# Kernel optimization log

Measured on AMD Instinct MI355X. Metric: run time of the kernel, lower is better.

Reference implementation:

```python
import jax, jax.numpy as jnp
import numpy as np

T, B, D, S, H, OUT = 365, 2048, 32, 27, 256, 1

def _glorot(key, shape):
    fan_in, fan_out = shape[1], shape[0]
    std = jnp.sqrt(2.0 / (fan_in + fan_out))
    return std * jax.random.normal(key, shape, dtype=jnp.float32)

def setup_inputs() -> dict:
    key = jax.random.key(0)
    ks = jax.random.split(key, 9)
    x_dd = jax.random.normal(ks[0], (T, B, D), dtype=jnp.float32)
    x_s = jax.random.normal(ks[1], (B, S), dtype=jnp.float32)
    weight_ih = _glorot(ks[2], (3 * H, D))
    weight_hh = _glorot(ks[3], (3 * H, H))
    bias = jnp.zeros((3 * H,), dtype=jnp.float32)
    w_in = _glorot(ks[4], (H, S))
    b_in = jnp.zeros((H,), dtype=jnp.float32)
    w_dense = _glorot(ks[5], (OUT, H))
    b_dense = jnp.zeros((OUT,), dtype=jnp.float32)
    return {"x_dd": x_dd, "x_s": x_s, "weight_ih": weight_ih,
            "weight_hh": weight_hh, "bias": bias, "w_in": w_in,
            "b_in": b_in, "w_dense": w_dense, "b_dense": b_dense}

def reference(x_dd, x_s, weight_ih, weight_hh, bias, w_in, b_in, w_dense, b_dense):
    # static input gate, computed once per sample: (B, H)
    i = jax.nn.sigmoid(x_s @ w_in.T + b_in)
    # precompute input projections for all timesteps: (T, B, 3H)
    x_proj = jnp.einsum('tbd,gd->tbg', x_dd, weight_ih) + bias

    def step(state, xp):
        h, c = state
        gates = xp + h @ weight_hh.T  # (B, 3H)
        f, g, o = jnp.split(gates, 3, axis=-1)
        f = jax.nn.sigmoid(f)
        g = jnp.tanh(g)
        o = jax.nn.sigmoid(o)
        c = f * c + i * g
        h = o * jnp.tanh(c)
        return (h, c), None

    init = (jnp.zeros((B, H), dtype=x_dd.dtype), jnp.zeros((B, H), dtype=x_dd.dtype))
    (h_final, _), _ = jax.lax.scan(step, init, x_proj)
    return h_final @ w_dense.T + b_dense  # (B, OUT)
```

## Files before the change

### kernel.cpp

```cpp
#include <hip/hip_runtime.h>

#define TT   365
#define BTOT 2048
#define DIN  32
#define SIN  27
#define HD   256
#define G3   768
#define BLOCK 512
#define ZBUF 4608
#define XOFF 4096
#define WIHL_OFF 9216
#define WHH7_OFF (WIHL_OFF + G3*64)
#define SMEM_SZ  (WHH7_OFF + G3*64)
#define L2E  1.442695040888963f

#define WS_WIH  (G3*HD*2)
#define WS_BIAS (WS_WIH + G3*DIN*2)

typedef float  f32x4  __attribute__((ext_vector_type(4)));
typedef short  bf16x8 __attribute__((ext_vector_type(8)));
typedef unsigned int u32x2 __attribute__((ext_vector_type(2)));

__device__ __forceinline__ unsigned short f2bf(float f) {
  unsigned u = __builtin_bit_cast(unsigned, f);
  u += 0x7fffu + ((u >> 16) & 1u);
  return (unsigned short)(u >> 16);
}
__device__ __forceinline__ float bf2f(unsigned short u) {
  unsigned v = ((unsigned)u) << 16;
  return __builtin_bit_cast(float, v);
}

__global__ void prep_kernel(const float* __restrict__ whh, const float* __restrict__ wih,
                            const float* __restrict__ bias,
                            unsigned short* __restrict__ whh_bf,
                            unsigned short* __restrict__ wih_bf,
                            float* __restrict__ bias_s) {
  int stride = gridDim.x * blockDim.x;
  int i0 = blockIdx.x * blockDim.x + threadIdx.x;
  for (int i = i0; i < G3 * HD; i += stride) {
    int row = i >> 8;
    float s = (row >= HD && row < 2 * HD) ? 2.0f * L2E : L2E;
    whh_bf[i] = f2bf(whh[i] * s);
  }
  for (int i = i0; i < G3 * DIN; i += stride) {
    int row = i >> 5;
    float s = (row >= HD && row < 2 * HD) ? 2.0f * L2E : L2E;
    wih_bf[i] = f2bf(wih[i] * s);
  }
  for (int i = i0; i < G3; i += stride) {
    float s = (i >= HD && i < 2 * HD) ? 2.0f * L2E : L2E;
    bias_s[i] = bias[i] * s;
  }
}

__global__ void __launch_bounds__(BLOCK, 2)
ealstm_kernel(const float* __restrict__ x_dd, const float* __restrict__ x_s,
              const float* __restrict__ w_in, const float* __restrict__ b_in,
              const float* __restrict__ w_dense, const float* __restrict__ b_dense,
              const unsigned short* __restrict__ whh_bf,
              const unsigned short* __restrict__ wih_bf,
              const float* __restrict__ bias_s,
              float* __restrict__ out) {
  __shared__ __attribute__((aligned(16))) char sm[SMEM_SZ];
  char* zb    = sm;
  char* wihl  = sm + WIHL_OFF;
  char* whh7l = sm + WHH7_OFF;

  const int tid  = threadIdx.x;
  const int b0   = blockIdx.x * 8;
  const int w    = tid >> 6;
  const int lane = tid & 63;
  const int m    = lane & 15;
  const int q    = lane >> 4;
  const int b    = m & 7;
  const int half = m >> 3;

  for (int i = tid; i < G3 * 4; i += BLOCK) {
    int row = i >> 2, qq = i & 3;
    int rot = ((qq + ((row >> 1) & 3)) & 3) << 4;
    *(bf16x8*)(wihl + row * 64 + rot)  = *(const bf16x8*)(wih_bf + row * DIN + qq * 8);
    *(bf16x8*)(whh7l + row * 64 + rot) =
        *(const bf16x8*)(whh_bf + (size_t)row * HD + 7 * 32 + qq * 8);
  }
  if (tid < 256) *(f32x4*)(zb + tid * 16) = f32x4{0.f, 0.f, 0.f, 0.f};

  const bool xthr = tid < 256;
  const int xr_ = (tid >> 5) & 7, xd = tid & 31;
  const int xso = XOFF + xr_ * 64 + ((((xd >> 3) + (xr_ >> 1)) & 3) << 4) + (xd & 7) * 2;
  const float* xq = x_dd + (size_t)(b0 + xr_) * DIN + xd;
  if (xthr) *(unsigned short*)(zb + xso) = f2bf(xq[0]);
  xq += (size_t)BTOT * DIN;

  const int sb0 = w * 16;
  int sbs[6];
  bf16x8 wr[6][7];
  #pragma unroll
  for (int s = 0; s < 6; ++s) {
    int sbase = sb0 + (s >= 3 ? 128 : 0) + (s % 3) * 256;
    sbs[s] = sbase;
    const unsigned short* wp = whh_bf + (size_t)(sbase + m) * HD + q * 8;
    #pragma unroll
    for (int kk = 0; kk < 7; ++kk) wr[s][kk] = *(const bf16x8*)(wp + kk * 32);
  }
  #pragma unroll
  for (int s = 0; s < 6; ++s)
    #pragma unroll
    for (int kk = 0; kk < 7; ++kk)
      asm volatile("" : "+v"(wr[s][kk]));

  const int j0 = sb0 + half * 128 + q * 4;
  float cst[4], ig[4];
  #pragma unroll
  for (int r = 0; r < 4; ++r) {
    int j = j0 + r;
    float a = b_in[j];
    const float* xr = x_s + (size_t)(b0 + b) * SIN;
    const float* wn = w_in + (size_t)j * SIN;
    #pragma unroll
    for (int ss = 0; ss < SIN; ++ss) a += xr[ss] * wn[ss];
    ig[r] = __builtin_amdgcn_rcpf(1.0f + __builtin_amdgcn_exp2f(-a * L2E));
    cst[r] = 0.0f;
  }

  const int swz = b << 4;
  const int wro = ((q + ((m >> 1) & 3)) & 3) << 4;
  const int xrd = XOFF + b * 64 + (((q + (b >> 1)) & 3) << 4);
  const int hrb = b * 512;
  const int hq  = q * 16;
  const int hw  = b * 512 + ((j0 * 2) ^ swz);
  const float* bfp = bias_s + j0;
  const float* bgp = bias_s + 256 + j0;
  const float* bop = bias_s + 512 + j0;

  const f32x4 z4 = f32x4{0.f, 0.f, 0.f, 0.f};
  __syncthreads();

  for (int t = 0; t < TT; ++t) {
    char* zc = zb + (t & 1) * ZBUF;
    char* zn = zb + ((t + 1) & 1) * ZBUF;

    float xv = 0.0f;
    if (xthr && t + 1 < TT) xv = xq[0];
    f32x4 bf4 = *(const f32x4*)bfp;
    f32x4 bg4 = *(const f32x4*)bgp;
    f32x4 bo4 = *(const f32x4*)bop;

    bf16x8 xf = *(const bf16x8*)(zc + xrd);
    f32x4 acc0, acc1, acc2, acc3, acc4, acc5;
    {
      bf16x8 w0 = *(const bf16x8*)(wihl + (sbs[0] + m) * 64 + wro);
      bf16x8 w1 = *(const bf16x8*)(wihl + (sbs[1] + m) * 64 + wro);
      bf16x8 w2 = *(const bf16x8*)(wihl + (sbs[2] + m) * 64 + wro);
      bf16x8 w3 = *(const bf16x8*)(wihl + (sbs[3] + m) * 64 + wro);
      bf16x8 w4 = *(const bf16x8*)(wihl + (sbs[4] + m) * 64 + wro);
      bf16x8 w5 = *(const bf16x8*)(wihl + (sbs[5] + m) * 64 + wro);
      acc0 = __builtin_amdgcn_mfma_f32_16x16x32_bf16(w0, xf, z4, 0, 0, 0);
      acc1 = __builtin_amdgcn_mfma_f32_16x16x32_bf16(w1, xf, z4, 0, 0, 0);
      acc2 = __builtin_amdgcn_mfma_f32_16x16x32_bf16(w2, xf, z4, 0, 0, 0);
      acc3 = __builtin_amdgcn_mfma_f32_16x16x32_bf16(w3, xf, z4, 0, 0, 0);
      acc4 = __builtin_amdgcn_mfma_f32_16x16x32_bf16(w4, xf, z4, 0, 0, 0);
      acc5 = __builtin_amdgcn_mfma_f32_16x16x32_bf16(w5, xf, z4, 0, 0, 0);
    }
    #pragma unroll
    for (int kk = 0; kk < 7; ++kk) {
      bf16x8 hf = *(const bf16x8*)(zc + hrb + ((kk * 64 + hq) ^ swz));
      acc0 = __builtin_amdgcn_mfma_f32_16x16x32_bf16(wr[0][kk], hf, acc0, 0, 0, 0);
      acc1 = __builtin_amdgcn_mfma_f32_16x16x32_bf16(wr[1][kk], hf, acc1, 0, 0, 0);
      acc2 = __builtin_amdgcn_mfma_f32_16x16x32_bf16(wr[2][kk], hf, acc2, 0, 0, 0);
      acc3 = __builtin_amdgcn_mfma_f32_16x16x32_bf16(wr[3][kk], hf, acc3, 0, 0, 0);
      acc4 = __builtin_amdgcn_mfma_f32_16x16x32_bf16(wr[4][kk], hf, acc4, 0, 0, 0);
      acc5 = __builtin_amdgcn_mfma_f32_16x16x32_bf16(wr[5][kk], hf, acc5, 0, 0, 0);
    }
    {
      bf16x8 hf = *(const bf16x8*)(zc + hrb + ((7 * 64 + hq) ^ swz));
      bf16x8 u0 = *(const bf16x8*)(whh7l + (sbs[0] + m) * 64 + wro);
      bf16x8 u1 = *(const bf16x8*)(whh7l + (sbs[1] + m) * 64 + wro);
      bf16x8 u2 = *(const bf16x8*)(whh7l + (sbs[2] + m) * 64 + wro);
      bf16x8 u3 = *(const bf16x8*)(whh7l + (sbs[3] + m) * 64 + wro);
      bf16x8 u4 = *(const bf16x8*)(whh7l + (sbs[4] + m) * 64 + wro);
      bf16x8 u5 = *(const bf16x8*)(whh7l + (sbs[5] + m) * 64 + wro);
      acc0 = __builtin_amdgcn_mfma_f32_16x16x32_bf16(u0, hf, acc0, 0, 0, 0);
      acc1 = __builtin_amdgcn_mfma_f32_16x16x32_bf16(u1, hf, acc1, 0, 0, 0);
      acc2 = __builtin_amdgcn_mfma_f32_16x16x32_bf16(u2, hf, acc2, 0, 0, 0);
      acc3 = __builtin_amdgcn_mfma_f32_16x16x32_bf16(u3, hf, acc3, 0, 0, 0);
      acc4 = __builtin_amdgcn_mfma_f32_16x16x32_bf16(u4, hf, acc4, 0, 0, 0);
      acc5 = __builtin_amdgcn_mfma_f32_16x16x32_bf16(u5, hf, acc5, 0, 0, 0);
    }

    float h0, h1, h2, h3;
    #pragma unroll
    for (int r = 0; r < 4; ++r) {
      float pf = (half ? acc3[r] : acc0[r]) + bf4[r];
      float pg = (half ? acc4[r] : acc1[r]) + bg4[r];
      float po = (half ? acc5[r] : acc2[r]) + bo4[r];
      float fg = __builtin_amdgcn_rcpf(1.0f + __builtin_amdgcn_exp2f(-pf));
      float gg = 1.0f - 2.0f * __builtin_amdgcn_rcpf(1.0f + __builtin_amdgcn_exp2f(pg));
      float og = __builtin_amdgcn_rcpf(1.0f + __builtin_amdgcn_exp2f(-po));
      float c  = fg * cst[r] + ig[r] * gg;
      cst[r] = c;
      float th = 1.0f - 2.0f * __builtin_amdgcn_rcpf(1.0f + __builtin_amdgcn_exp2f(c * (2.0f * L2E)));
      float hv = og * th;
      if (r == 0) h0 = hv; else if (r == 1) h1 = hv; else if (r == 2) h2 = hv; else h3 = hv;
    }
    unsigned pk0, pk1;
    asm("v_cvt_pk_bf16_f32 %0, %1, %2" : "=v"(pk0) : "v"(h0), "v"(h1));
    asm("v_cvt_pk_bf16_f32 %0, %1, %2" : "=v"(pk1) : "v"(h2), "v"(h3));
    u32x2 pk = u32x2{pk0, pk1};
    *(u32x2*)(zn + hw) = pk;

    if (xthr && t + 1 < TT) {
      *(unsigned short*)(zn + xso) = f2bf(xv);
      xq += (size_t)BTOT * DIN;
    }
    __syncthreads();
  }

  if (tid < 64) {
    const char* hb = zb + (TT & 1) * ZBUF;
    int row = tid >> 3, seg = tid & 7;
    float sum = 0.0f;
    #pragma unroll
    for (int jj = 0; jj < 32; ++jj) {
      int j = seg * 32 + jj;
      unsigned short hu = *(const unsigned short*)(hb + row * 512 + ((j * 2) ^ (row << 4)));
      sum += bf2f(hu) * w_dense[j];
    }
    sum += __shfl_xor(sum, 1, 64);
    sum += __shfl_xor(sum, 2, 64);
    sum += __shfl_xor(sum, 4, 64);
    if (seg == 0) out[b0 + row] = sum + b_dense[0];
  }
}

extern "C" void kernel_launch(void* const* d_in, const int* in_sizes, int n_in,
                              void* d_out, int out_size, void* d_ws, size_t ws_size,
                              hipStream_t stream) {
  (void)in_sizes; (void)n_in; (void)out_size; (void)ws_size;
  const float* x_dd = (const float*)d_in[0];
  const float* x_s  = (const float*)d_in[1];
  const float* wih  = (const float*)d_in[2];
  const float* whh  = (const float*)d_in[3];
  const float* bias = (const float*)d_in[4];
  const float* w_in = (const float*)d_in[5];
  const float* b_in = (const float*)d_in[6];
  const float* w_d  = (const float*)d_in[7];
  const float* b_d  = (const float*)d_in[8];
  float* out = (float*)d_out;
  unsigned char* ws = (unsigned char*)d_ws;

  unsigned short* whh_bf = (unsigned short*)ws;
  unsigned short* wih_bf = (unsigned short*)(ws + WS_WIH);
  float*          bias_s = (float*)(ws + WS_BIAS);

  prep_kernel<<<128, 256, 0, stream>>>(whh, wih, bias, whh_bf, wih_bf, bias_s);
  ealstm_kernel<<<BTOT / 8, BLOCK, 0, stream>>>(
      x_dd, x_s, w_in, b_in, w_d, b_d, whh_bf, wih_bf, bias_s, out);
}
```

Baseline: 527.9 us.

## Reorder gate MFMAs so f/g finish first and overlap cell update with o-gate

Reassigns weight slices so the f and g gate accumulators (acc0-3) are computed before the o gate (acc4-5), letting the cell-state update start while the o-gate MFMAs are still in flight. Biases are hoisted out of the time loop into registers. The LDS h swizzle is simplified to a 2-bit XOR with a precomputed base pointer, and the x store is moved earlier. This targets the serial latency of each recurrent step, at the cost of higher register pressure and a possible change in LDS bank-conflict behaviour.

Result: slower. 681.3 us (+29.1%).

```diff
diff --git a/kernel.cpp b/kernel.cpp
--- a/kernel.cpp
+++ b/kernel.cpp
@@ -97,7 +97,7 @@
   bf16x8 wr[6][7];
   #pragma unroll
   for (int s = 0; s < 6; ++s) {
-    int sbase = sb0 + (s >= 3 ? 128 : 0) + (s % 3) * 256;
+    int sbase = sb0 + (s >> 1) * 256 + (s & 1) * 128;
     sbs[s] = sbase;
     const unsigned short* wp = whh_bf + (size_t)(sbase + m) * HD + q * 8;
     #pragma unroll
@@ -123,15 +123,15 @@
     cst[r] = 0.0f;
   }
 
-  const int swz = b << 4;
-  const int wro = ((q + ((m >> 1) & 3)) & 3) << 4;
-  const int xrd = XOFF + b * 64 + (((q + (b >> 1)) & 3) << 4);
-  const int hrb = b * 512;
-  const int hq  = q * 16;
-  const int hw  = b * 512 + ((j0 * 2) ^ swz);
-  const float* bfp = bias_s + j0;
-  const float* bgp = bias_s + 256 + j0;
-  const float* bop = bias_s + 512 + j0;
+  const int swz2 = (b & 3) << 4;
+  const int wro  = ((q + ((m >> 1) & 3)) & 3) << 4;
+  const int xrd  = XOFF + b * 64 + (((q + (b >> 1)) & 3) << 4);
+  const int hbro = b * 512 + ((q * 16) ^ swz2);
+  const int hw   = b * 512 + ((j0 * 2) ^ swz2);
+
+  const f32x4 bf4 = *(const f32x4*)(bias_s + j0);
+  const f32x4 bg4 = *(const f32x4*)(bias_s + 256 + j0);
+  const f32x4 bo4 = *(const f32x4*)(bias_s + 512 + j0);
 
   const f32x4 z4 = f32x4{0.f, 0.f, 0.f, 0.f};
   __syncthreads();
@@ -142,64 +142,81 @@
 
     float xv = 0.0f;
     if (xthr && t + 1 < TT) xv = xq[0];
-    f32x4 bf4 = *(const f32x4*)bfp;
-    f32x4 bg4 = *(const f32x4*)bgp;
-    f32x4 bo4 = *(const f32x4*)bop;
-
+
+    const char* hb = zc + hbro;
     bf16x8 xf = *(const bf16x8*)(zc + xrd);
     f32x4 acc0, acc1, acc2, acc3, acc4, acc5;
+
     {
       bf16x8 w0 = *(const bf16x8*)(wihl + (sbs[0] + m) * 64 + wro);
       bf16x8 w1 = *(const bf16x8*)(wihl + (sbs[1] + m) * 64 + wro);
       bf16x8 w2 = *(const bf16x8*)(wihl + (sbs[2] + m) * 64 + wro);
       bf16x8 w3 = *(const bf16x8*)(wihl + (sbs[3] + m) * 64 + wro);
-      bf16x8 w4 = *(const bf16x8*)(wihl + (sbs[4] + m) * 64 + wro);
-      bf16x8 w5 = *(const bf16x8*)(wihl + (sbs[5] + m) * 64 + wro);
       acc0 = __builtin_amdgcn_mfma_f32_16x16x32_bf16(w0, xf, z4, 0, 0, 0);
       acc1 = __builtin_amdgcn_mfma_f32_16x16x32_bf16(w1, xf, z4, 0, 0, 0);
       acc2 = __builtin_amdgcn_mfma_f32_16x16x32_bf16(w2, xf, z4, 0, 0, 0);
       acc3 = __builtin_amdgcn_mfma_f32_16x16x32_bf16(w3, xf, z4, 0, 0, 0);
-      acc4 = __builtin_amdgcn_mfma_f32_16x16x32_bf16(w4, xf, z4, 0, 0, 0);
-      acc5 = __builtin_amdgcn_mfma_f32_16x16x32_bf16(w5, xf, z4, 0, 0, 0);
     }
     #pragma unroll
     for (int kk = 0; kk < 7; ++kk) {
-      bf16x8 hf = *(const bf16x8*)(zc + hrb + ((kk * 64 + hq) ^ swz));
+      bf16x8 hf = *(const bf16x8*)(hb + kk * 64);
       acc0 = __builtin_amdgcn_mfma_f32_16x16x32_bf16(wr[0][kk], hf, acc0, 0, 0, 0);
       acc1 = __builtin_amdgcn_mfma_f32_16x16x32_bf16(wr[1][kk], hf, acc1, 0, 0, 0);
       acc2 = __builtin_amdgcn_mfma_f32_16x16x32_bf16(wr[2][kk], hf, acc2, 0, 0, 0);
       acc3 = __builtin_amdgcn_mfma_f32_16x16x32_bf16(wr[3][kk], hf, acc3, 0, 0, 0);
-      acc4 = __builtin_amdgcn_mfma_f32_16x16x32_bf16(wr[4][kk], hf, acc4, 0, 0, 0);
-      acc5 = __builtin_amdgcn_mfma_f32_16x16x32_bf16(wr[5][kk], hf, acc5, 0, 0, 0);
-    }
-    {
-      bf16x8 hf = *(const bf16x8*)(zc + hrb + ((7 * 64 + hq) ^ swz));
+    }
+    {
+      bf16x8 hf = *(const bf16x8*)(hb + 7 * 64);
       bf16x8 u0 = *(const bf16x8*)(whh7l + (sbs[0] + m) * 64 + wro);
       bf16x8 u1 = *(const bf16x8*)(whh7l + (sbs[1] + m) * 64 + wro);
       bf16x8 u2 = *(const bf16x8*)(whh7l + (sbs[2] + m) * 64 + wro);
       bf16x8 u3 = *(const bf16x8*)(whh7l + (sbs[3] + m) * 64 + wro);
-      bf16x8 u4 = *(const bf16x8*)(whh7l + (sbs[4] + m) * 64 + wro);
-      bf16x8 u5 = *(const bf16x8*)(whh7l + (sbs[5] + m) * 64 + wro);
       acc0 = __builtin_amdgcn_mfma_f32_16x16x32_bf16(u0, hf, acc0, 0, 0, 0);
       acc1 = __builtin_amdgcn_mfma_f32_16x16x32_bf16(u1, hf, acc1, 0, 0, 0);
       acc2 = __builtin_amdgcn_mfma_f32_16x16x32_bf16(u2, hf, acc2, 0, 0, 0);
       acc3 = __builtin_amdgcn_mfma_f32_16x16x32_bf16(u3, hf, acc3, 0, 0, 0);
+    }
+
+    {
+      bf16x8 w4 = *(const bf16x8*)(wihl + (sbs[4] + m) * 64 + wro);
+      bf16x8 w5 = *(const bf16x8*)(wihl + (sbs[5] + m) * 64 + wro);
+      acc4 = __builtin_amdgcn_mfma_f32_16x16x32_bf16(w4, xf, z4, 0, 0, 0);
+      acc5 = __builtin_amdgcn_mfma_f32_16x16x32_bf16(w5, xf, z4, 0, 0, 0);
+    }
+    #pragma unroll
+    for (int kk = 0; kk < 7; ++kk) {
+      bf16x8 hf = *(const bf16x8*)(hb + kk * 64);
+      acc4 = __builtin_amdgcn_mfma_f32_16x16x32_bf16(wr[4][kk], hf, acc4, 0, 0, 0);
+      acc5 = __builtin_amdgcn_mfma_f32_16x16x32_bf16(wr[5][kk], hf, acc5, 0, 0, 0);
+    }
+    {
+      bf16x8 hf = *(const bf16x8*)(hb + 7 * 64);
+      bf16x8 u4 = *(const bf16x8*)(whh7l + (sbs[4] + m) * 64 + wro);
+      bf16x8 u5 = *(const bf16x8*)(whh7l + (sbs[5] + m) * 64 + wro);
       acc4 = __builtin_amdgcn_mfma_f32_16x16x32_bf16(u4, hf, acc4, 0, 0, 0);
       acc5 = __builtin_amdgcn_mfma_f32_16x16x32_bf16(u5, hf, acc5, 0, 0, 0);
     }
 
-    float h0, h1, h2, h3;
+    if (xthr && t + 1 < TT) {
+      *(unsigned short*)(zn + xso) = f2bf(xv);
+      xq += (size_t)BTOT * DIN;
+    }
+
     #pragma unroll
     for (int r = 0; r < 4; ++r) {
-      float pf = (half ? acc3[r] : acc0[r]) + bf4[r];
-      float pg = (half ? acc4[r] : acc1[r]) + bg4[r];
-      float po = (half ? acc5[r] : acc2[r]) + bo4[r];
+      float pf = (half ? acc1[r] : acc0[r]) + bf4[r];
+      float pg = (half ? acc3[r] : acc2[r]) + bg4[r];
       float fg = __builtin_amdgcn_rcpf(1.0f + __builtin_amdgcn_exp2f(-pf));
       float gg = 1.0f - 2.0f * __builtin_amdgcn_rcpf(1.0f + __builtin_amdgcn_exp2f(pg));
+      cst[r] = fg * cst[r] + ig[r] * gg;
+    }
+
+    float h0, h1, h2, h3;
+    #pragma unroll
+    for (int r = 0; r < 4; ++r) {
+      float po = (half ? acc5[r] : acc4[r]) + bo4[r];
       float og = __builtin_amdgcn_rcpf(1.0f + __builtin_amdgcn_exp2f(-po));
-      float c  = fg * cst[r] + ig[r] * gg;
-      cst[r] = c;
-      float th = 1.0f - 2.0f * __builtin_amdgcn_rcpf(1.0f + __builtin_amdgcn_exp2f(c * (2.0f * L2E)));
+      float th = 1.0f - 2.0f * __builtin_amdgcn_rcpf(1.0f + __builtin_amdgcn_exp2f(cst[r] * (2.0f * L2E)));
       float hv = og * th;
       if (r == 0) h0 = hv; else if (r == 1) h1 = hv; else if (r == 2) h2 = hv; else h3 = hv;
     }
@@ -209,10 +226,6 @@
     u32x2 pk = u32x2{pk0, pk1};
     *(u32x2*)(zn + hw) = pk;
 
-    if (xthr && t + 1 < TT) {
-      *(unsigned short*)(zn + xso) = f2bf(xv);
-      xq += (size_t)BTOT * DIN;
-    }
     __syncthreads();
   }
 
@@ -223,7 +236,7 @@
     #pragma unroll
     for (int jj = 0; jj < 32; ++jj) {
       int j = seg * 32 + jj;
-      unsigned short hu = *(const unsigned short*)(hb + row * 512 + ((j * 2) ^ (row << 4)));
+      unsigned short hu = *(const unsigned short*)(hb + row * 512 + ((j * 2) ^ ((row & 3) << 4)));
       sum += bf2f(hu) * w_dense[j];
     }
     sum += __shfl_xor(sum, 1, 64);
```

## Load x per lane into registers and hoist next-step input MFMAs before barrier

Applied to the files above, without the earlier changes.

Each lane now loads its own x_dd fragment straight from global memory into registers and converts it to bf16, so x no longer goes through shared memory. The input-projection MFMAs for step t+1 are issued at the end of step t, before the barrier, so they overlap with the sync and shrink the critical path at the start of the next step. The gate math is also split so the x load can be issued between computing c and computing h. The cost is an extra global load per lane per step and more live registers across the barrier.

After: 624.3 us. 1.18x slower.

```diff
diff --git a/kernel.cpp b/kernel.cpp
--- a/kernel.cpp
+++ b/kernel.cpp
@@ -7,9 +7,8 @@
 #define HD   256
 #define G3   768
 #define BLOCK 512
-#define ZBUF 4608
-#define XOFF 4096
-#define WIHL_OFF 9216
+#define ZBUF 4096
+#define WIHL_OFF 8192
 #define WHH7_OFF (WIHL_OFF + G3*64)
 #define SMEM_SZ  (WHH7_OFF + G3*64)
 #define L2E  1.442695040888963f
@@ -20,6 +19,7 @@
 typedef float  f32x4  __attribute__((ext_vector_type(4)));
 typedef short  bf16x8 __attribute__((ext_vector_type(8)));
 typedef unsigned int u32x2 __attribute__((ext_vector_type(2)));
+typedef unsigned int u32x4 __attribute__((ext_vector_type(4)));
 
 __device__ __forceinline__ unsigned short f2bf(float f) {
   unsigned u = __builtin_bit_cast(unsigned, f);
@@ -29,6 +29,15 @@
 __device__ __forceinline__ float bf2f(unsigned short u) {
   unsigned v = ((unsigned)u) << 16;
   return __builtin_bit_cast(float, v);
+}
+__device__ __forceinline__ bf16x8 cvt8(f32x4 a, f32x4 c) {
+  unsigned c0, c1, c2, c3;
+  asm("v_cvt_pk_bf16_f32 %0, %1, %2" : "=v"(c0) : "v"(a[0]), "v"(a[1]));
+  asm("v_cvt_pk_bf16_f32 %0, %1, %2" : "=v"(c1) : "v"(a[2]), "v"(a[3]));
+  asm("v_cvt_pk_bf16_f32 %0, %1, %2" : "=v"(c2) : "v"(c[0]), "v"(c[1]));
+  asm("v_cvt_pk_bf16_f32 %0, %1, %2" : "=v"(c3) : "v"(c[2]), "v"(c[3]));
+  u32x4 u = u32x4{c0, c1, c2, c3};
+  return __builtin_bit_cast(bf16x8, u);
 }
 
 __global__ void prep_kernel(const float* __restrict__ whh, const float* __restrict__ wih,
@@ -85,12 +94,10 @@
   }
   if (tid < 256) *(f32x4*)(zb + tid * 16) = f32x4{0.f, 0.f, 0.f, 0.f};
 
-  const bool xthr = tid < 256;
-  const int xr_ = (tid >> 5) & 7, xd = tid & 31;
-  const int xso = XOFF + xr_ * 64 + ((((xd >> 3) + (xr_ >> 1)) & 3) << 4) + (xd & 7) * 2;
-  const float* xq = x_dd + (size_t)(b0 + xr_) * DIN + xd;
-  if (xthr) *(unsigned short*)(zb + xso) = f2bf(xq[0]);
-  xq += (size_t)BTOT * DIN;
+  const float* xp = x_dd + ((size_t)(b0 + b)) * DIN + q * 8;
+  f32x4 xa = *(const f32x4*)xp;
+  f32x4 xc = *(const f32x4*)(xp + 4);
+  xp += (size_t)BTOT * DIN;
 
   const int sb0 = w * 16;
   int sbs[6];
@@ -125,7 +132,6 @@
 
   const int swz = b << 4;
   const int wro = ((q + ((m >> 1) & 3)) & 3) << 4;
-  const int xrd = XOFF + b * 64 + (((q + (b >> 1)) & 3) << 4);
   const int hrb = b * 512;
   const int hq  = q * 16;
   const int hw  = b * 512 + ((j0 * 2) ^ swz);
@@ -136,32 +142,32 @@
   const f32x4 z4 = f32x4{0.f, 0.f, 0.f, 0.f};
   __syncthreads();
 
+  f32x4 acc0, acc1, acc2, acc3, acc4, acc5;
+  {
+    bf16x8 xf = cvt8(xa, xc);
+    bf16x8 w0 = *(const bf16x8*)(wihl + (sbs[0] + m) * 64 + wro);
+    bf16x8 w1 = *(const bf16x8*)(wihl + (sbs[1] + m) * 64 + wro);
+    bf16x8 w2 = *(const bf16x8*)(wihl + (sbs[2] + m) * 64 + wro);
+    bf16x8 w3 = *(const bf16x8*)(wihl + (sbs[3] + m) * 64 + wro);
+    bf16x8 w4 = *(const bf16x8*)(wihl + (sbs[4] + m) * 64 + wro);
+    bf16x8 w5 = *(const bf16x8*)(wihl + (sbs[5] + m) * 64 + wro);
+    acc0 = __builtin_amdgcn_mfma_f32_16x16x32_bf16(w0, xf, z4, 0, 0, 0);
+    acc1 = __builtin_amdgcn_mfma_f32_16x16x32_bf16(w1, xf, z4, 0, 0, 0);
+    acc2 = __builtin_amdgcn_mfma_f32_16x16x32_bf16(w2, xf, z4, 0, 0, 0);
+    acc3 = __builtin_amdgcn_mfma_f32_16x16x32_bf16(w3, xf, z4, 0, 0, 0);
+    acc4 = __builtin_amdgcn_mfma_f32_16x16x32_bf16(w4, xf, z4, 0, 0, 0);
+    acc5 = __builtin_amdgcn_mfma_f32_16x16x32_bf16(w5, xf, z4, 0, 0, 0);
+  }
+
   for (int t = 0; t < TT; ++t) {
     char* zc = zb + (t & 1) * ZBUF;
     char* zn = zb + ((t + 1) & 1) * ZBUF;
-
-    float xv = 0.0f;
-    if (xthr && t + 1 < TT) xv = xq[0];
+    const bool more = (t + 1 < TT);
+
     f32x4 bf4 = *(const f32x4*)bfp;
     f32x4 bg4 = *(const f32x4*)bgp;
     f32x4 bo4 = *(const f32x4*)bop;
 
-    bf16x8 xf = *(const bf16x8*)(zc + xrd);
-    f32x4 acc0, acc1, acc2, acc3, acc4, acc5;
-    {
-      bf16x8 w0 = *(const bf16x8*)(wihl + (sbs[0] + m) * 64 + wro);
-      bf16x8 w1 = *(const bf16x8*)(wihl + (sbs[1] + m) * 64 + wro);
-      bf16x8 w2 = *(const bf16x8*)(wihl + (sbs[2] + m) * 64 + wro);
-      bf16x8 w3 = *(const bf16x8*)(wihl + (sbs[3] + m) * 64 + wro);
-      bf16x8 w4 = *(const bf16x8*)(wihl + (sbs[4] + m) * 64 + wro);
-      bf16x8 w5 = *(const bf16x8*)(wihl + (sbs[5] + m) * 64 + wro);
-      acc0 = __builtin_amdgcn_mfma_f32_16x16x32_bf16(w0, xf, z4, 0, 0, 0);
-      acc1 = __builtin_amdgcn_mfma_f32_16x16x32_bf16(w1, xf, z4, 0, 0, 0);
-      acc2 = __builtin_amdgcn_mfma_f32_16x16x32_bf16(w2, xf, z4, 0, 0, 0);
-      acc3 = __builtin_amdgcn_mfma_f32_16x16x32_bf16(w3, xf, z4, 0, 0, 0);
-      acc4 = __builtin_amdgcn_mfma_f32_16x16x32_bf16(w4, xf, z4, 0, 0, 0);
-      acc5 = __builtin_amdgcn_mfma_f32_16x16x32_bf16(w5, xf, z4, 0, 0, 0);
-    }
     #pragma unroll
     for (int kk = 0; kk < 7; ++kk) {
       bf16x8 hf = *(const bf16x8*)(zc + hrb + ((kk * 64 + hq) ^ swz));
@@ -188,18 +194,27 @@
       acc5 = __builtin_amdgcn_mfma_f32_16x16x32_bf16(u5, hf, acc5, 0, 0, 0);
     }
 
-    float h0, h1, h2, h3;
     #pragma unroll
     for (int r = 0; r < 4; ++r) {
       float pf = (half ? acc3[r] : acc0[r]) + bf4[r];
       float pg = (half ? acc4[r] : acc1[r]) + bg4[r];
-      float po = (half ? acc5[r] : acc2[r]) + bo4[r];
       float fg = __builtin_amdgcn_rcpf(1.0f + __builtin_amdgcn_exp2f(-pf));
       float gg = 1.0f - 2.0f * __builtin_amdgcn_rcpf(1.0f + __builtin_amdgcn_exp2f(pg));
+      cst[r] = fg * cst[r] + ig[r] * gg;
+    }
+
+    if (more) {
+      xa = *(const f32x4*)xp;
+      xc = *(const f32x4*)(xp + 4);
+      xp += (size_t)BTOT * DIN;
+    }
+
+    float h0, h1, h2, h3;
+    #pragma unroll
+    for (int r = 0; r < 4; ++r) {
+      float po = (half ? acc5[r] : acc2[r]) + bo4[r];
       float og = __builtin_amdgcn_rcpf(1.0f + __builtin_amdgcn_exp2f(-po));
-      float c  = fg * cst[r] + ig[r] * gg;
-      cst[r] = c;
-      float th = 1.0f - 2.0f * __builtin_amdgcn_rcpf(1.0f + __builtin_amdgcn_exp2f(c * (2.0f * L2E)));
+      float th = 1.0f - 2.0f * __builtin_amdgcn_rcpf(1.0f + __builtin_amdgcn_exp2f(cst[r] * (2.0f * L2E)));
       float hv = og * th;
       if (r == 0) h0 = hv; else if (r == 1) h1 = hv; else if (r == 2) h2 = hv; else h3 = hv;
     }
@@ -209,9 +224,20 @@
     u32x2 pk = u32x2{pk0, pk1};
     *(u32x2*)(zn + hw) = pk;
 
-    if (xthr && t + 1 < TT) {
-      *(unsigned short*)(zn + xso) = f2bf(xv);
-      xq += (size_t)BTOT * DIN;
+    if (more) {
+      bf16x8 xf = cvt8(xa, xc);
+      bf16x8 w0 = *(const bf16x8*)(wihl + (sbs[0] + m) * 64 + wro);
+      bf16x8 w1 = *(const bf16x8*)(wihl + (sbs[1] + m) * 64 + wro);
+      bf16x8 w2 = *(const bf16x8*)(wihl + (sbs[2] + m) * 64 + wro);
+      bf16x8 w3 = *(const bf16x8*)(wihl + (sbs[3] + m) * 64 + wro);
+      bf16x8 w4 = *(const bf16x8*)(wihl + (sbs[4] + m) * 64 + wro);
+      bf16x8 w5 = *(const bf16x8*)(wihl + (sbs[5] + m) * 64 + wro);
+      acc0 = __builtin_amdgcn_mfma_f32_16x16x32_bf16(w0, xf, z4, 0, 0, 0);
+      acc1 = __builtin_amdgcn_mfma_f32_16x16x32_bf16(w1, xf, z4, 0, 0, 0);
+      acc2 = __builtin_amdgcn_mfma_f32_16x16x32_bf16(w2, xf, z4, 0, 0, 0);
+      acc3 = __builtin_amdgcn_mfma_f32_16x16x32_bf16(w3, xf, z4, 0, 0, 0);
+      acc4 = __builtin_amdgcn_mfma_f32_16x16x32_bf16(w4, xf, z4, 0, 0, 0);
+      acc5 = __builtin_amdgcn_mfma_f32_16x16x32_bf16(w5, xf, z4, 0, 0, 0);
     }
     __syncthreads();
   }
```
